# Kernel optimization log

Hardware: AMD Instinct MI355X
Metric: run time of the kernel (lower is better)

## Reference

```python
import jax, jax.numpy as jnp
import numpy as np

B, S, D, H = 4, 2048, 512, 4
HD = D // H
EPS = 1e-5


def layer_norm(x, gamma, beta):
    mu = jnp.mean(x, axis=-1, keepdims=True)
    var = jnp.mean(jnp.square(x - mu), axis=-1, keepdims=True)
    return (x - mu) * jax.lax.rsqrt(var + EPS) * gamma + beta


def setup_inputs() -> dict:
    key = jax.random.key(0)
    ks = jax.random.split(key, 16)
    s_in = 1.0 / np.sqrt(D)
    s_ex = 1.0 / np.sqrt(2 * D)
    return {
        "input_states": jax.random.normal(ks[0], (B, S, D), jnp.float32),
        "positions": jax.random.normal(ks[1], (B, S, 3), jnp.float32),
        "W_expand": jax.random.uniform(ks[2], (D, 2 * D), jnp.float32, -s_in, s_in),
        "b_expand": jax.random.uniform(ks[3], (2 * D,), jnp.float32, -s_in, s_in),
        "W_squeeze": jax.random.uniform(ks[4], (2 * D, D), jnp.float32, -s_ex, s_ex),
        "b_squeeze": jax.random.uniform(ks[5], (D,), jnp.float32, -s_ex, s_ex),
        "gamma": jnp.ones((D,), jnp.float32),
        "beta": jnp.zeros((D,), jnp.float32),
        "Wq": jax.random.uniform(ks[6], (D, D), jnp.float32, -s_in, s_in),
        "bq": jax.random.uniform(ks[7], (D,), jnp.float32, -s_in, s_in),
        "Wk": jax.random.uniform(ks[8], (D, D), jnp.float32, -s_in, s_in),
        "bk": jax.random.uniform(ks[9], (D,), jnp.float32, -s_in, s_in),
        "Wv": jax.random.uniform(ks[10], (D, D), jnp.float32, -s_in, s_in),
        "bv": jax.random.uniform(ks[11], (D,), jnp.float32, -s_in, s_in),
        "alpha": jnp.float32(0.1),
    }


def reference(input_states, positions, W_expand, b_expand, W_squeeze, b_squeeze,
              gamma, beta, Wq, bq, Wk, bk, Wv, bv, alpha):
    # FFN (expand -> relu -> squeeze) + residual + LayerNorm
    h = jax.nn.relu(input_states @ W_expand + b_expand)
    squeezed = h @ W_squeeze + b_squeeze
    se = layer_norm(input_states + squeezed, gamma, beta)

    # q/k/v projections, split heads: [B,H,S,HD]
    q = (se @ Wq + bq).reshape(B, S, H, HD).transpose(0, 2, 1, 3)
    k = (se @ Wk + bk).reshape(B, S, H, HD).transpose(0, 2, 1, 3)
    v = (se @ Wv + bv).reshape(B, S, H, HD).transpose(0, 2, 1, 3)

    scores = jnp.einsum('bhid,bhjd->bhij', q, k) / np.sqrt(HD)

    # squared pairwise distance bias: ||pi||^2 + ||pj||^2 - 2 pi.pj, broadcast over heads
    sq = jnp.sum(positions * positions, axis=-1)  # [B,S]
    dist2 = sq[:, :, None] + sq[:, None, :] - 2.0 * jnp.einsum('bic,bjc->bij', positions, positions)
    dist2 = jnp.maximum(dist2, 0.0)
    scores = scores - alpha * dist2[:, None, :, :]

    w = jax.nn.softmax(scores, axis=-1)
    ctx = jnp.einsum('bhij,bhjd->bhid', w, v)
    ctx = ctx.transpose(0, 2, 1, 3).reshape(B, S, D)

    # same LayerNorm params reused (self.norm applied twice in original)
    return layer_norm(se + ctx, gamma, beta)
```

## Files before the change

kernel.cpp:

```cpp
#include <hip/hip_runtime.h>

typedef __bf16 bf16_t;
typedef __attribute__((ext_vector_type(8))) __bf16 bf16x8;
typedef __attribute__((ext_vector_type(4))) __bf16 bf16x4;
typedef __attribute__((ext_vector_type(4))) float f32x4;
typedef __attribute__((ext_vector_type(16))) float f32x16;

constexpr int Bc = 4, Sc = 2048, Dc = 512, Hc = 4, HDc = 128;
constexpr int Mrows = Bc * Sc;

__device__ inline void gl2lds(const void* g, void* l) {
  __builtin_amdgcn_global_load_lds(
      (__attribute__((address_space(1))) void*)g,
      (__attribute__((address_space(3))) void*)l, 16, 0, 0);
}

__global__ __launch_bounds__(256) void prep_k(
    const float* __restrict__ X, bf16_t* __restrict__ xb,
    const float* __restrict__ pos, const float* __restrict__ alphap,
    bf16_t* __restrict__ Qbg, bf16_t* __restrict__ Kbg,
    const float* __restrict__ We, bf16_t* __restrict__ wtE,
    const float* __restrict__ Ws, bf16_t* __restrict__ wtS,
    const float* __restrict__ Wq, const float* __restrict__ Wk,
    const float* __restrict__ Wv, bf16_t* __restrict__ wtQKV) {
  const int bid = blockIdx.x;
  if (bid < 2048) {
    const long i = ((long)bid * 256 + threadIdx.x) * 8;
    const float4 a = *(const float4*)(X + i);
    const float4 c = *(const float4*)(X + i + 4);
    bf16x8 o;
    o[0] = (bf16_t)a.x; o[1] = (bf16_t)a.y; o[2] = (bf16_t)a.z; o[3] = (bf16_t)a.w;
    o[4] = (bf16_t)c.x; o[5] = (bf16_t)c.y; o[6] = (bf16_t)c.z; o[7] = (bf16_t)c.w;
    *(bf16x8*)(xb + i) = o;
    return;
  }
  if (bid < 2080) {
    const float ap = alphap[0] * 11.313708498984761f;
    const int i = (bid - 2048) * 256 + threadIdx.x;
    const int b = i >> 11, s = i & 2047;
    const float x = pos[(long)i * 3], y = pos[(long)i * 3 + 1], z = pos[(long)i * 3 + 2];
    const float m2 = -ap * (x * x + y * y + z * z);
    bf16x8 qlo = {}, klo = {}, zer = {};
    qlo[0] = (bf16_t)(2.f * ap * x); qlo[1] = (bf16_t)(2.f * ap * y);
    qlo[2] = (bf16_t)(2.f * ap * z); qlo[3] = (bf16_t)1.0f;
    klo[0] = (bf16_t)x; klo[1] = (bf16_t)y; klo[2] = (bf16_t)z; klo[3] = (bf16_t)m2;
    *(bf16x8*)(Qbg + (long)i * 16) = qlo;
    *(bf16x8*)(Qbg + (long)i * 16 + 8) = zer;
    const int t = s >> 6, kh = (s >> 5) & 1, key = s & 31;
    const long kb = ((long)(b * 32 + t) * 2 + kh) * 512 + key * 8;
    *(bf16x8*)(Kbg + kb) = klo;
    *(bf16x8*)(Kbg + kb + 256) = zer;
    return;
  }
  __shared__ float tile[32][33];
  const float* src; bf16_t* dst; int K, N, local;
  if (bid < 2592)      { src = We; dst = wtE; K = 512;  N = 1024; local = bid - 2080; }
  else if (bid < 3104) { src = Ws; dst = wtS; K = 1024; N = 512;  local = bid - 2592; }
  else if (bid < 3360) { src = Wq; dst = wtQKV;          K = 512; N = 512; local = bid - 3104; }
  else if (bid < 3616) { src = Wk; dst = wtQKV + 262144; K = 512; N = 512; local = bid - 3360; }
  else                 { src = Wv; dst = wtQKV + 524288; K = 512; N = 512; local = bid - 3616; }
  const int nb = N / 32;
  const int n0 = (local % nb) * 32, k0 = (local / nb) * 32;
  const int tx = threadIdx.x & 31, ty = threadIdx.x >> 5;
#pragma unroll
  for (int i = 0; i < 4; i++)
    tile[ty + i * 8][tx] = src[(long)(k0 + ty + i * 8) * N + n0 + tx];
  __syncthreads();
#pragma unroll
  for (int i = 0; i < 4; i++)
    dst[(long)(n0 + ty + i * 8) * K + k0 + tx] = (bf16_t)tile[tx][ty + i * 8];
}

template <int OMODE, int TN, int NB>
__global__ __launch_bounds__(256, (TN == 128) ? 2 : 3) void gemm128_k(
    const bf16_t* __restrict__ A, const bf16_t* __restrict__ Bt,
    const float* __restrict__ bias0, const float* __restrict__ bias1,
    const float* __restrict__ bias2, void* __restrict__ out0,
    void* __restrict__ out1, void* __restrict__ out2, int N, int K) {
  __shared__ bf16_t As[2][128 * 64];
  __shared__ bf16_t Bs[2][TN * 64];
  constexpr int MT = (TN == 128) ? 4 : 2;
  constexpr int BI = (TN == 128) ? 4 : 2;
  constexpr int MW = (TN == 128) ? 64 : 32;
  const int t = threadIdx.x;
  const int p = blockIdx.x;
  const int slot = p >> 3;
  const int by = (p & 7) + 8 * (slot / NB);
  const int bx = slot % NB;
  const int n0 = bx * TN, m0 = by * 128;
  const int lane = t & 63, wave = t >> 6;
  const int quad = lane >> 4, ln = lane & 15;
  const int wm = (TN == 128) ? (wave >> 1) : wave;
  const int wn = (TN == 128) ? (wave & 1) : 0;
  const int l8 = lane >> 3, g = lane & 7;
  const bf16_t* aseg = A + (long)(m0 + wave * 32 + l8) * K + (g ^ l8) * 8;
  const bf16_t* bseg = Bt + (long)(n0 + wave * (BI * 8) + l8) * K + (g ^ l8) * 8;
  auto stage = [&](int buf, int k0) {
#pragma unroll
    for (int i = 0; i < 4; i++)
      gl2lds(aseg + (long)i * 8 * K + k0, &As[buf][(wave * 32 + i * 8) * 64]);
#pragma unroll
    for (int i = 0; i < BI; i++)
      gl2lds(bseg + (long)i * 8 * K + k0, &Bs[buf][(wave * BI * 8 + i * 8) * 64]);
  };
  f32x4 acc[MT][4] = {};
  stage(0, 0);
  const int niter = K / 64;
  for (int it = 0; it < niter; it++) {
    const int cur = it & 1;
    __syncthreads();
    if (it + 1 < niter) stage(1 - cur, (it + 1) * 64);
#pragma unroll
    for (int kc = 0; kc < 2; kc++) {
      bf16x8 af[MT], bfr[4];
#pragma unroll
      for (int mt = 0; mt < MT; mt++)
        af[mt] = *(const bf16x8*)&As[cur][(wm * MW + mt * 16 + ln) * 64 +
                                          (((kc * 4 + quad) ^ (ln & 7)) * 8)];
#pragma unroll
      for (int nt = 0; nt < 4; nt++)
        bfr[nt] = *(const bf16x8*)&Bs[cur][(wn * 64 + nt * 16 + ln) * 64 +
                                           (((kc * 4 + quad) ^ (ln & 7)) * 8)];
#pragma unroll
      for (int mt = 0; mt < MT; mt++)
#pragma unroll
        for (int nt = 0; nt < 4; nt++)
          acc[mt][nt] = __builtin_amdgcn_mfma_f32_16x16x32_bf16(af[mt], bfr[nt],
                                                                acc[mt][nt], 0, 0, 0);
    }
  }
#pragma unroll
  for (int nt = 0; nt < 4; nt++) {
    const int gcol = n0 + wn * 64 + nt * 16 + ln;
    if constexpr (OMODE == 0 || OMODE == 1) {
      const float bv = bias0[gcol];
      bf16_t* o = (bf16_t*)out0;
#pragma unroll
      for (int mt = 0; mt < MT; mt++)
#pragma unroll
        for (int r = 0; r < 4; r++) {
          const int grow = m0 + wm * MW + mt * 16 + quad * 4 + r;
          float vv = acc[mt][nt][r] + bv;
          if constexpr (OMODE == 0) vv = vv > 0.f ? vv : 0.f;
          o[(long)grow * N + gcol] = (bf16_t)vv;
        }
    } else {
      const int which = gcol >> 9, n = gcol & 511;
      const int hh = n >> 7, hd = n & 127;
      const float bv = (which == 0 ? bias0 : which == 1 ? bias1 : bias2)[n];
      bf16_t* o = (bf16_t*)(which == 0 ? out0 : which == 1 ? out1 : out2);
#pragma unroll
      for (int mt = 0; mt < MT; mt++)
#pragma unroll
        for (int r = 0; r < 4; r++) {
          const int grow = m0 + wm * MW + mt * 16 + quad * 4 + r;
          const int b = grow >> 11, s = grow & 2047;
          const float vv = acc[mt][nt][r] + bv;
          long idx;
          if (which == 0) {
            idx = ((long)((b * Hc + hh) * Sc + s)) * HDc + hd;
          } else if (which == 1) {
            const int tt = s >> 6, kh = (s >> 5) & 1, key = s & 31;
            const int c = hd >> 4, lk = key + 32 * ((hd >> 3) & 1), j = hd & 7;
            idx = ((((long)((b * Hc + hh) * 32 + tt) * 2 + kh) * 8 + c) * 64 + lk) * 8 + j;
          } else {
            const int tt = s >> 6, ht2 = hd >> 5, kc2 = (s & 63) >> 4;
            const int kl = s & 15;
            const int klp = (kl & 3) | ((kl & 4) << 1) | ((kl & 8) >> 1);
            const int lk = (hd & 31) + 32 * (klp >> 3), j = klp & 7;
            idx = ((((long)((b * Hc + hh) * 32 + tt) * 4 + ht2) * 4 + kc2) * 64 + lk) * 8 + j;
          }
          o[idx] = (bf16_t)vv;
        }
    }
  }
}

template <int AF32, int OF32>
__global__ __launch_bounds__(256) void ln_k(const void* __restrict__ xa,
                                            const bf16_t* __restrict__ xb,
                                            const float* __restrict__ gamma,
                                            const float* __restrict__ beta,
                                            void* __restrict__ out) {
  const int wave = threadIdx.x >> 6, lane = threadIdx.x & 63;
  const long row = (long)blockIdx.x * 4 + wave;
  const int col0 = lane * 8;
  float vv[8];
  float s = 0.f, s2 = 0.f;
  const bf16x8 vb = *(const bf16x8*)(xb + row * Dc + col0);
  if constexpr (AF32) {
    const float* a = (const float*)xa + row * Dc + col0;
    const float4 a0 = *(const float4*)a;
    const float4 a1 = *(const float4*)(a + 4);
    const float xs[8] = {a0.x, a0.y, a0.z, a0.w, a1.x, a1.y, a1.z, a1.w};
#pragma unroll
    for (int j = 0; j < 8; j++) vv[j] = xs[j] + (float)vb[j];
  } else {
    const bf16x8 va = *(const bf16x8*)((const bf16_t*)xa + row * Dc + col0);
#pragma unroll
    for (int j = 0; j < 8; j++) vv[j] = (float)va[j] + (float)vb[j];
  }
#pragma unroll
  for (int j = 0; j < 8; j++) { s += vv[j]; s2 += vv[j] * vv[j]; }
#pragma unroll
  for (int off = 1; off < 64; off <<= 1) {
    s += __shfl_xor(s, off, 64);
    s2 += __shfl_xor(s2, off, 64);
  }
  const float mu = s * (1.f / Dc);
  const float var = s2 * (1.f / Dc) - mu * mu;
  const float rstd = rsqrtf(var + 1e-5f);
  const float4 g0 = *(const float4*)(gamma + col0);
  const float4 g1 = *(const float4*)(gamma + col0 + 4);
  const float4 b0 = *(const float4*)(beta + col0);
  const float4 b1 = *(const float4*)(beta + col0 + 4);
  const float gs[8] = {g0.x, g0.y, g0.z, g0.w, g1.x, g1.y, g1.z, g1.w};
  const float bs[8] = {b0.x, b0.y, b0.z, b0.w, b1.x, b1.y, b1.z, b1.w};
  if constexpr (OF32) {
    float* o = (float*)out + row * Dc + col0;
    float4 o0, o1;
    o0.x = (vv[0] - mu) * rstd * gs[0] + bs[0];
    o0.y = (vv[1] - mu) * rstd * gs[1] + bs[1];
    o0.z = (vv[2] - mu) * rstd * gs[2] + bs[2];
    o0.w = (vv[3] - mu) * rstd * gs[3] + bs[3];
    o1.x = (vv[4] - mu) * rstd * gs[4] + bs[4];
    o1.y = (vv[5] - mu) * rstd * gs[5] + bs[5];
    o1.z = (vv[6] - mu) * rstd * gs[6] + bs[6];
    o1.w = (vv[7] - mu) * rstd * gs[7] + bs[7];
    *(float4*)o = o0; *(float4*)(o + 4) = o1;
  } else {
    bf16x8 ob;
#pragma unroll
    for (int j = 0; j < 8; j++) ob[j] = (bf16_t)((vv[j] - mu) * rstd * gs[j] + bs[j]);
    *(bf16x8*)((bf16_t*)out + row * Dc + col0) = ob;
  }
}

__global__ __launch_bounds__(256, 2) void attn_k(const bf16_t* __restrict__ q,
                                                 const bf16_t* __restrict__ Kg,
                                                 const bf16_t* __restrict__ Vg,
                                                 const bf16_t* __restrict__ Qbg,
                                                 const bf16_t* __restrict__ Kbg,
                                                 bf16_t* __restrict__ ctx) {
  __shared__ float Oc[8192];
  __shared__ float RsD[4][32];
  const int t = threadIdx.x;
  const int p = blockIdx.x;
  const int qt = (p >> 3) & 31;
  const int gg = (p & 7) + 8 * (p >> 8);
  const int h = gg & 3, b = gg >> 2;
  const int q0 = qt * 64;
  const int wave = t >> 6, lane = t & 63;
  const int l31 = lane & 31, hb = lane >> 5;
  const int rh = wave & 1, kh = wave >> 1;
  const float scale_l2 = 1.4426950408889634f * 0.08838834764831845f;

  bf16x8 qf[8], qbf;
  const long qrow = (long)((b * Hc + h) * Sc + q0 + rh * 32 + l31);
#pragma unroll
  for (int c = 0; c < 8; c++)
    qf[c] = *(const bf16x8*)(q + qrow * HDc + c * 16 + hb * 8);
  qbf = *(const bf16x8*)(Qbg + (long)(b * Sc + q0 + rh * 32 + l31) * 16 + hb * 8);

  const bf16_t* kfb = Kg + (long)((b * Hc + h) * 32) * 8192 + (kh * 8) * 512 + lane * 8;
  const bf16_t* vfb = Vg + (long)((b * Hc + h) * 32) * 8192 + kh * 1024 + lane * 8;
  const bf16_t* kbb = Kbg + (long)(b * 32) * 1024 + kh * 512 + lane * 8;

  bf16x8 kr[8], vr[8], kbr;
#pragma unroll
  for (int c = 0; c < 8; c++) kr[c] = *(const bf16x8*)(kfb + c * 512);
  kbr = *(const bf16x8*)(kbb);
#pragma unroll
  for (int i = 0; i < 8; i++)
    vr[i] = *(const bf16x8*)(vfb + (i >> 1) * 2048 + (i & 1) * 512);

  float rsl = 0.f;
  f32x16 accT[4] = {};

  for (int kt = 0; kt < 32; kt++) {
    f32x16 sa = {}, sb = {};
    __builtin_amdgcn_s_setprio(1);
#pragma unroll
    for (int c = 0; c < 4; c++)
      sa = __builtin_amdgcn_mfma_f32_32x32x16_bf16(kr[c], qf[c], sa, 0, 0, 0);
#pragma unroll
    for (int c = 4; c < 8; c++)
      sb = __builtin_amdgcn_mfma_f32_32x32x16_bf16(kr[c], qf[c], sb, 0, 0, 0);
    sb = __builtin_amdgcn_mfma_f32_32x32x16_bf16(kbr, qbf, sb, 0, 0, 0);
    __builtin_amdgcn_s_setprio(0);
    __builtin_amdgcn_sched_barrier(0);
    {
      const long noff = (long)(kt + 1) * 8192;
#pragma unroll
      for (int c = 0; c < 8; c++)
        kr[c] = *(const bf16x8*)(kfb + noff + c * 512);
      kbr = *(const bf16x8*)(kbb + (long)(kt + 1) * 1024);
    }
    const f32x16 sacc = sa + sb;
    float pe[16];
#pragma unroll
    for (int i = 0; i < 16; i++) {
      pe[i] = __builtin_amdgcn_exp2f(sacc[i] * scale_l2);
      rsl += pe[i];
    }
    bf16x8 pf0, pf1;
#pragma unroll
    for (int j = 0; j < 8; j++) { pf0[j] = (bf16_t)pe[j]; pf1[j] = (bf16_t)pe[8 + j]; }
    __builtin_amdgcn_s_setprio(1);
#pragma unroll
    for (int ht = 0; ht < 4; ht++) {
      accT[ht] = __builtin_amdgcn_mfma_f32_32x32x16_bf16(vr[2 * ht], pf0, accT[ht], 0, 0, 0);
      accT[ht] = __builtin_amdgcn_mfma_f32_32x32x16_bf16(vr[2 * ht + 1], pf1, accT[ht], 0, 0, 0);
    }
    __builtin_amdgcn_s_setprio(0);
    __builtin_amdgcn_sched_barrier(0);
    {
      const long noff = (long)(kt + 1) * 8192;
#pragma unroll
      for (int i = 0; i < 8; i++)
        vr[i] = *(const bf16x8*)(vfb + noff + (i >> 1) * 2048 + (i & 1) * 512);
    }
  }
  __syncthreads();

  rsl += __shfl_xor(rsl, 32, 64);
  if (hb == 0) RsD[wave][l31] = rsl;
  if (kh == 1) {
#pragma unroll
    for (int ht = 0; ht < 4; ht++)
#pragma unroll
      for (int r = 0; r < 16; r++) {
        const int hdp = (r & 3) + 8 * (r >> 2) + 4 * hb;
        Oc[(ht * 32 + hdp) * 64 + rh * 32 + l31] = accT[ht][r];
      }
  }
  __syncthreads();
  if (kh == 0) {
    const float rinv = 1.f / (RsD[wave][l31] + RsD[wave + 2][l31]);
    const long orow = (long)(b * Sc + q0 + rh * 32 + l31);
#pragma unroll
    for (int ht = 0; ht < 4; ht++)
#pragma unroll
      for (int g2 = 0; g2 < 4; g2++) {
        bf16x4 ov;
#pragma unroll
        for (int r0 = 0; r0 < 4; r0++) {
          const int hdp = r0 + 8 * g2 + 4 * hb;
          ov[r0] = (bf16_t)((accT[ht][g2 * 4 + r0] +
                             Oc[(ht * 32 + hdp) * 64 + rh * 32 + l31]) * rinv);
        }
        *(bf16x4*)(ctx + orow * Dc + h * HDc + ht * 32 + 8 * g2 + 4 * hb) = ov;
      }
  }
}

constexpr size_t SQB_OFF = 0;
constexpr size_t SEB_OFF = 8388608;
constexpr size_t Q_OFF = 16777216;
constexpr size_t K_OFF = 25165824;
constexpr size_t V_OFF = 33554432;
constexpr size_t XB_OFF = Q_OFF;
constexpr size_t H_OFF = K_OFF;
constexpr size_t QBG_OFF = 41943040;
constexpr size_t KBG_OFF = QBG_OFF + 262144;
constexpr size_t WTE_OFF = KBG_OFF + 262144;
constexpr size_t WTS_OFF = WTE_OFF + 1048576;
constexpr size_t WTQKV_OFF = WTS_OFF + 1048576;

extern "C" void kernel_launch(void* const* d_in, const int* in_sizes, int n_in,
                              void* d_out, int out_size, void* d_ws, size_t ws_size,
                              hipStream_t stream) {
  const float* X = (const float*)d_in[0];
  const float* pos = (const float*)d_in[1];
  const float* W_expand = (const float*)d_in[2];
  const float* b_expand = (const float*)d_in[3];
  const float* W_squeeze = (const float*)d_in[4];
  const float* b_squeeze = (const float*)d_in[5];
  const float* gamma = (const float*)d_in[6];
  const float* beta = (const float*)d_in[7];
  const float* Wq = (const float*)d_in[8];
  const float* bq = (const float*)d_in[9];
  const float* Wk = (const float*)d_in[10];
  const float* bk = (const float*)d_in[11];
  const float* Wv = (const float*)d_in[12];
  const float* bv = (const float*)d_in[13];
  const float* alphap = (const float*)d_in[14];

  char* ws = (char*)d_ws;
  bf16_t* sqb = (bf16_t*)(ws + SQB_OFF);
  bf16_t* ctxb = (bf16_t*)(ws + SQB_OFF);
  bf16_t* seb = (bf16_t*)(ws + SEB_OFF);
  bf16_t* qbg = (bf16_t*)(ws + QBG_OFF);
  bf16_t* kbg = (bf16_t*)(ws + KBG_OFF);
  bf16_t* qb = (bf16_t*)(ws + Q_OFF);
  bf16_t* kb = (bf16_t*)(ws + K_OFF);
  bf16_t* vb = (bf16_t*)(ws + V_OFF);
  bf16_t* xbb = (bf16_t*)(ws + XB_OFF);
  bf16_t* hb = (bf16_t*)(ws + H_OFF);
  bf16_t* wtE = (bf16_t*)(ws + WTE_OFF);
  bf16_t* wtS = (bf16_t*)(ws + WTS_OFF);
  bf16_t* wtQKV = (bf16_t*)(ws + WTQKV_OFF);

  prep_k<<<3872, 256, 0, stream>>>(X, xbb, pos, alphap, qbg, kbg,
                                   W_expand, wtE, W_squeeze, wtS, Wq, Wk, Wv, wtQKV);
  gemm128_k<0, 128, 8><<<512, 256, 0, stream>>>(
      xbb, wtE, b_expand, nullptr, nullptr, hb, nullptr, nullptr, 1024, 512);
  gemm128_k<1, 64, 8><<<512, 256, 0, stream>>>(
      hb, wtS, b_squeeze, nullptr, nullptr, sqb, nullptr, nullptr, 512, 1024);
  ln_k<1, 0><<<Mrows / 4, 256, 0, stream>>>(X, sqb, gamma, beta, seb);
  gemm128_k<2, 128, 12><<<768, 256, 0, stream>>>(
      seb, wtQKV, bq, bk, bv, qb, kb, vb, 1536, 512);
  attn_k<<<512, 256, 0, stream>>>(qb, kb, vb, qbg, kbg, ctxb);
  ln_k<0, 1><<<Mrows / 4, 256, 0, stream>>>(seb, ctxb, gamma, beta, (float*)d_out);

  (void)in_sizes; (void)n_in; (void)out_size; (void)ws_size;
}
```

Measured before the change: 215.7 us.

## Split attention key range across two wave groups with 512-thread blocks

Doubles the attention block to 512 threads, with a second group of four waves handling the second half of the key tiles (split-K over the sequence). Partial output accumulators and row sums are reduced through enlarged shared memory before the existing cross-half reduction and normalization. This is meant to raise parallelism and latency hiding given only 512 blocks on many CUs, at the cost of doubled LDS use, extra barriers and a reduction step. Launch bounds now request 4 blocks of 512 threads per CU, which tightens the register budget and may cause spills.

```diff
diff --git a/kernel.cpp b/kernel.cpp
--- a/kernel.cpp
+++ b/kernel.cpp
@@ -236,14 +236,14 @@
   }
 }
 
-__global__ __launch_bounds__(256, 2) void attn_k(const bf16_t* __restrict__ q,
+__global__ __launch_bounds__(512, 4) void attn_k(const bf16_t* __restrict__ q,
                                                  const bf16_t* __restrict__ Kg,
                                                  const bf16_t* __restrict__ Vg,
                                                  const bf16_t* __restrict__ Qbg,
                                                  const bf16_t* __restrict__ Kbg,
                                                  bf16_t* __restrict__ ctx) {
-  __shared__ float Oc[8192];
-  __shared__ float RsD[4][32];
+  __shared__ float Oc[16384];
+  __shared__ float RsD[8][32];
   const int t = threadIdx.x;
   const int p = blockIdx.x;
   const int qt = (p >> 3) & 31;
@@ -252,7 +252,7 @@
   const int q0 = qt * 64;
   const int wave = t >> 6, lane = t & 63;
   const int l31 = lane & 31, hb = lane >> 5;
-  const int rh = wave & 1, kh = wave >> 1;
+  const int rh = wave & 1, kh = (wave >> 1) & 1, ks = wave >> 2;
   const float scale_l2 = 1.4426950408889634f * 0.08838834764831845f;
 
   bf16x8 qf[8], qbf;
@@ -262,9 +262,11 @@
     qf[c] = *(const bf16x8*)(q + qrow * HDc + c * 16 + hb * 8);
   qbf = *(const bf16x8*)(Qbg + (long)(b * Sc + q0 + rh * 32 + l31) * 16 + hb * 8);
 
-  const bf16_t* kfb = Kg + (long)((b * Hc + h) * 32) * 8192 + (kh * 8) * 512 + lane * 8;
-  const bf16_t* vfb = Vg + (long)((b * Hc + h) * 32) * 8192 + kh * 1024 + lane * 8;
-  const bf16_t* kbb = Kbg + (long)(b * 32) * 1024 + kh * 512 + lane * 8;
+  const bf16_t* kfb = Kg + (long)((b * Hc + h) * 32 + ks * 16) * 8192 +
+                      (kh * 8) * 512 + lane * 8;
+  const bf16_t* vfb = Vg + (long)((b * Hc + h) * 32 + ks * 16) * 8192 +
+                      kh * 1024 + lane * 8;
+  const bf16_t* kbb = Kbg + (long)(b * 32 + ks * 16) * 1024 + kh * 512 + lane * 8;
 
   bf16x8 kr[8], vr[8], kbr;
 #pragma unroll
@@ -277,7 +279,7 @@
   float rsl = 0.f;
   f32x16 accT[4] = {};
 
-  for (int kt = 0; kt < 32; kt++) {
+  for (int kt = 0; kt < 16; kt++) {
     f32x16 sa = {}, sb = {};
     __builtin_amdgcn_s_setprio(1);
 #pragma unroll
@@ -321,11 +323,28 @@
         vr[i] = *(const bf16x8*)(vfb + noff + (i >> 1) * 2048 + (i & 1) * 512);
     }
   }
-  __syncthreads();
 
   rsl += __shfl_xor(rsl, 32, 64);
   if (hb == 0) RsD[wave][l31] = rsl;
-  if (kh == 1) {
+  if (ks == 1) {
+    float* dst = &Oc[(wave - 4) * 4096];
+#pragma unroll
+    for (int ht = 0; ht < 4; ht++)
+#pragma unroll
+      for (int r = 0; r < 16; r++)
+        dst[(ht * 16 + r) * 64 + lane] = accT[ht][r];
+  }
+  __syncthreads();
+  if (ks == 0) {
+    const float* src = &Oc[wave * 4096];
+#pragma unroll
+    for (int ht = 0; ht < 4; ht++)
+#pragma unroll
+      for (int r = 0; r < 16; r++)
+        accT[ht][r] += src[(ht * 16 + r) * 64 + lane];
+  }
+  __syncthreads();
+  if (ks == 0 && kh == 1) {
 #pragma unroll
     for (int ht = 0; ht < 4; ht++)
 #pragma unroll
@@ -335,8 +354,9 @@
       }
   }
   __syncthreads();
-  if (kh == 0) {
-    const float rinv = 1.f / (RsD[wave][l31] + RsD[wave + 2][l31]);
+  if (ks == 0 && kh == 0) {
+    const float rinv = 1.f / (RsD[rh][l31] + RsD[rh + 2][l31] +
+                              RsD[rh + 4][l31] + RsD[rh + 6][l31]);
     const long orow = (long)(b * Sc + q0 + rh * 32 + l31);
 #pragma unroll
     for (int ht = 0; ht < 4; ht++)
@@ -410,7 +430,7 @@
   ln_k<1, 0><<<Mrows / 4, 256, 0, stream>>>(X, sqb, gamma, beta, seb);
   gemm128_k<2, 128, 12><<<768, 256, 0, stream>>>(
       seb, wtQKV, bq, bk, bv, qb, kb, vb, 1536, 512);
-  attn_k<<<512, 256, 0, stream>>>(qb, kb, vb, qbg, kbg, ctxb);
+  attn_k<<<512, 512, 0, stream>>>(qb, kb, vb, qbg, kbg, ctxb);
   ln_k<0, 1><<<Mrows / 4, 256, 0, stream>>>(seb, ctxb, gamma, beta, (float*)d_out);
 
   (void)in_sizes; (void)n_in; (void)out_size; (void)ws_size;
```

After: 539.4 us. 2.5x slower.

## Split attention PV head dimension across twice as many waves per block

Applied to the files above, without the earlier changes.

The attention kernel moves from 256 to 512 threads per block. Each pair of waves now splits the 128-wide head dimension of the PV product, so each wave keeps half the output accumulators and loads only its half of V. The explicit register prefetch of the next K/V tile is removed; loads are issued inline right before each MFMA. This lowers register pressure and raises wave occupancy so more waves can hide latency, but every wave in a pair repeats the QK^T score MFMAs and exp work, and the tiles are no longer software-pipelined.

```diff
diff --git a/kernel.cpp b/kernel.cpp
--- a/kernel.cpp
+++ b/kernel.cpp
@@ -236,14 +236,14 @@
   }
 }
 
-__global__ __launch_bounds__(256, 2) void attn_k(const bf16_t* __restrict__ q,
+__global__ __launch_bounds__(512, 4) void attn_k(const bf16_t* __restrict__ q,
                                                  const bf16_t* __restrict__ Kg,
                                                  const bf16_t* __restrict__ Vg,
                                                  const bf16_t* __restrict__ Qbg,
                                                  const bf16_t* __restrict__ Kbg,
                                                  bf16_t* __restrict__ ctx) {
   __shared__ float Oc[8192];
-  __shared__ float RsD[4][32];
+  __shared__ float RsD[8][32];
   const int t = threadIdx.x;
   const int p = blockIdx.x;
   const int qt = (p >> 3) & 31;
@@ -252,7 +252,7 @@
   const int q0 = qt * 64;
   const int wave = t >> 6, lane = t & 63;
   const int l31 = lane & 31, hb = lane >> 5;
-  const int rh = wave & 1, kh = wave >> 1;
+  const int rh = wave & 1, hh = (wave >> 1) & 1, kh = wave >> 2;
   const float scale_l2 = 1.4426950408889634f * 0.08838834764831845f;
 
   bf16x8 qf[8], qbf;
@@ -263,40 +263,27 @@
   qbf = *(const bf16x8*)(Qbg + (long)(b * Sc + q0 + rh * 32 + l31) * 16 + hb * 8);
 
   const bf16_t* kfb = Kg + (long)((b * Hc + h) * 32) * 8192 + (kh * 8) * 512 + lane * 8;
-  const bf16_t* vfb = Vg + (long)((b * Hc + h) * 32) * 8192 + kh * 1024 + lane * 8;
+  const bf16_t* vfb = Vg + (long)((b * Hc + h) * 32) * 8192 + (hh * 2) * 2048 +
+                      kh * 1024 + lane * 8;
   const bf16_t* kbb = Kbg + (long)(b * 32) * 1024 + kh * 512 + lane * 8;
 
-  bf16x8 kr[8], vr[8], kbr;
-#pragma unroll
-  for (int c = 0; c < 8; c++) kr[c] = *(const bf16x8*)(kfb + c * 512);
-  kbr = *(const bf16x8*)(kbb);
-#pragma unroll
-  for (int i = 0; i < 8; i++)
-    vr[i] = *(const bf16x8*)(vfb + (i >> 1) * 2048 + (i & 1) * 512);
-
   float rsl = 0.f;
-  f32x16 accT[4] = {};
+  f32x16 accT[2] = {};
 
   for (int kt = 0; kt < 32; kt++) {
-    f32x16 sa = {}, sb = {};
+    const bf16_t* kt_k = kfb + (long)kt * 8192;
+    f32x16 sacc = {};
     __builtin_amdgcn_s_setprio(1);
 #pragma unroll
-    for (int c = 0; c < 4; c++)
-      sa = __builtin_amdgcn_mfma_f32_32x32x16_bf16(kr[c], qf[c], sa, 0, 0, 0);
-#pragma unroll
-    for (int c = 4; c < 8; c++)
-      sb = __builtin_amdgcn_mfma_f32_32x32x16_bf16(kr[c], qf[c], sb, 0, 0, 0);
-    sb = __builtin_amdgcn_mfma_f32_32x32x16_bf16(kbr, qbf, sb, 0, 0, 0);
+    for (int c = 0; c < 8; c++) {
+      const bf16x8 kr = *(const bf16x8*)(kt_k + c * 512);
+      sacc = __builtin_amdgcn_mfma_f32_32x32x16_bf16(kr, qf[c], sacc, 0, 0, 0);
+    }
+    {
+      const bf16x8 kbr = *(const bf16x8*)(kbb + (long)kt * 1024);
+      sacc = __builtin_amdgcn_mfma_f32_32x32x16_bf16(kbr, qbf, sacc, 0, 0, 0);
+    }
     __builtin_amdgcn_s_setprio(0);
-    __builtin_amdgcn_sched_barrier(0);
-    {
-      const long noff = (long)(kt + 1) * 8192;
-#pragma unroll
-      for (int c = 0; c < 8; c++)
-        kr[c] = *(const bf16x8*)(kfb + noff + c * 512);
-      kbr = *(const bf16x8*)(kbb + (long)(kt + 1) * 1024);
-    }
-    const f32x16 sacc = sa + sb;
     float pe[16];
 #pragma unroll
     for (int i = 0; i < 16; i++) {
@@ -306,50 +293,48 @@
     bf16x8 pf0, pf1;
 #pragma unroll
     for (int j = 0; j < 8; j++) { pf0[j] = (bf16_t)pe[j]; pf1[j] = (bf16_t)pe[8 + j]; }
+    const bf16_t* vt = vfb + (long)kt * 8192;
     __builtin_amdgcn_s_setprio(1);
 #pragma unroll
-    for (int ht = 0; ht < 4; ht++) {
-      accT[ht] = __builtin_amdgcn_mfma_f32_32x32x16_bf16(vr[2 * ht], pf0, accT[ht], 0, 0, 0);
-      accT[ht] = __builtin_amdgcn_mfma_f32_32x32x16_bf16(vr[2 * ht + 1], pf1, accT[ht], 0, 0, 0);
+    for (int ht2 = 0; ht2 < 2; ht2++) {
+      const bf16x8 v0 = *(const bf16x8*)(vt + ht2 * 2048);
+      accT[ht2] = __builtin_amdgcn_mfma_f32_32x32x16_bf16(v0, pf0, accT[ht2], 0, 0, 0);
+      const bf16x8 v1 = *(const bf16x8*)(vt + ht2 * 2048 + 512);
+      accT[ht2] = __builtin_amdgcn_mfma_f32_32x32x16_bf16(v1, pf1, accT[ht2], 0, 0, 0);
     }
     __builtin_amdgcn_s_setprio(0);
-    __builtin_amdgcn_sched_barrier(0);
-    {
-      const long noff = (long)(kt + 1) * 8192;
-#pragma unroll
-      for (int i = 0; i < 8; i++)
-        vr[i] = *(const bf16x8*)(vfb + noff + (i >> 1) * 2048 + (i & 1) * 512);
-    }
   }
   __syncthreads();
 
   rsl += __shfl_xor(rsl, 32, 64);
   if (hb == 0) RsD[wave][l31] = rsl;
   if (kh == 1) {
-#pragma unroll
-    for (int ht = 0; ht < 4; ht++)
-#pragma unroll
-      for (int r = 0; r < 16; r++) {
-        const int hdp = (r & 3) + 8 * (r >> 2) + 4 * hb;
-        Oc[(ht * 32 + hdp) * 64 + rh * 32 + l31] = accT[ht][r];
-      }
+    float* dst = &Oc[(rh + 2 * hh) * 2048];
+#pragma unroll
+    for (int ht2 = 0; ht2 < 2; ht2++)
+#pragma unroll
+      for (int r = 0; r < 16; r++)
+        dst[(ht2 * 16 + r) * 64 + lane] = accT[ht2][r];
   }
   __syncthreads();
   if (kh == 0) {
-    const float rinv = 1.f / (RsD[wave][l31] + RsD[wave + 2][l31]);
+    const float* src = &Oc[(rh + 2 * hh) * 2048];
+#pragma unroll
+    for (int ht2 = 0; ht2 < 2; ht2++)
+#pragma unroll
+      for (int r = 0; r < 16; r++)
+        accT[ht2][r] += src[(ht2 * 16 + r) * 64 + lane];
+    const float rinv = 1.f / (RsD[wave][l31] + RsD[wave + 4][l31]);
     const long orow = (long)(b * Sc + q0 + rh * 32 + l31);
 #pragma unroll
-    for (int ht = 0; ht < 4; ht++)
+    for (int ht2 = 0; ht2 < 2; ht2++)
 #pragma unroll
       for (int g2 = 0; g2 < 4; g2++) {
         bf16x4 ov;
 #pragma unroll
-        for (int r0 = 0; r0 < 4; r0++) {
-          const int hdp = r0 + 8 * g2 + 4 * hb;
-          ov[r0] = (bf16_t)((accT[ht][g2 * 4 + r0] +
-                             Oc[(ht * 32 + hdp) * 64 + rh * 32 + l31]) * rinv);
-        }
-        *(bf16x4*)(ctx + orow * Dc + h * HDc + ht * 32 + 8 * g2 + 4 * hb) = ov;
+        for (int r0 = 0; r0 < 4; r0++)
+          ov[r0] = (bf16_t)(accT[ht2][g2 * 4 + r0] * rinv);
+        *(bf16x4*)(ctx + orow * Dc + h * HDc + (hh * 2 + ht2) * 32 + 8 * g2 + 4 * hb) = ov;
       }
   }
 }
@@ -410,7 +395,7 @@
   ln_k<1, 0><<<Mrows / 4, 256, 0, stream>>>(X, sqb, gamma, beta, seb);
   gemm128_k<2, 128, 12><<<768, 256, 0, stream>>>(
       seb, wtQKV, bq, bk, bv, qb, kb, vb, 1536, 512);
-  attn_k<<<512, 256, 0, stream>>>(qb, kb, vb, qbg, kbg, ctxb);
+  attn_k<<<512, 512, 0, stream>>>(qb, kb, vb, qbg, kbg, ctxb);
   ln_k<0, 1><<<Mrows / 4, 256, 0, stream>>>(seb, ctxb, gamma, beta, (float*)d_out);
 
   (void)in_sizes; (void)n_in; (void)out_size; (void)ws_size;
```

Result: slower. 260.9 us (+20.9%).
